# Kernel tuning notes

Hardware: AMD Instinct MI355X
Metric: run time of the kernel (lower is better)

Reference implementation:

```python
import jax, jax.numpy as jnp
import numpy as np

N_NODES = 50000
N_EDGES = 500000
N_REL = 8
D = 128        # input_dim
A_DIM = 64     # attention_dim
D_OUT = 128    # output_dim


def setup_inputs() -> dict:
    key = jax.random.key(0)
    ks = jax.random.split(key, 10)
    h = jax.random.normal(ks[0], (N_NODES, D), jnp.float32)
    # relation gate tables: [R, 2*D, D]; first D rows act on dst (subject), last D on src (object)
    relations = jax.random.normal(ks[1], (N_REL, 2 * D, D), jnp.float32) * 0.05
    rel_attention = jax.random.normal(ks[2], (N_REL, A_DIM), jnp.float32) * 0.05
    W_a = jax.random.normal(ks[3], (A_DIM, 2 * D), jnp.float32) * 0.05
    b_a = jnp.zeros((A_DIM,), jnp.float32)
    W_lin = jax.random.normal(ks[4], (D_OUT, 2 * D), jnp.float32) * 0.05
    b_lin = jnp.zeros((D_OUT,), jnp.float32)
    src = jax.random.randint(ks[5], (N_EDGES,), 0, N_NODES, dtype=jnp.int32)
    dst = jax.random.randint(ks[6], (N_EDGES,), 0, N_NODES, dtype=jnp.int32)
    etype = jax.random.randint(ks[7], (N_EDGES,), 0, N_REL, dtype=jnp.int32)
    return {"h": h, "relations": relations, "rel_attention": rel_attention,
            "W_a": W_a, "b_a": b_a, "W_lin": W_lin, "b_lin": b_lin,
            "src": src, "dst": dst, "etype": etype}


def reference(h, relations, rel_attention, W_a, b_a, W_lin, b_lin, src, dst, etype):
    d = h.shape[-1]
    # --- gates: relation-indexed gather_mm (concat gate type) ---
    # Project every node through every relation once (R is small), then gather per edge.
    proj_dst = jnp.einsum('nd,rde->rne', h, relations[:, :d, :])   # [R, N, D] subject/dst side
    proj_src = jnp.einsum('nd,rde->rne', h, relations[:, d:, :])   # [R, N, D] object/src side
    gate = jax.nn.sigmoid(proj_dst[etype, dst] + proj_src[etype, src])  # [E, D]

    src_h = h[src]   # [E, D]
    dst_h = h[dst]   # [E, D]

    # --- gatv2 attention (predicates are zeroed in the module -> rel_attention[0]) ---
    a = jax.nn.leaky_relu(jnp.concatenate([dst_h, src_h], axis=-1) @ W_a.T + b_a)  # [E, A]
    score = (rel_attention[0] * a).sum(-1)  # [E]

    # --- edge_softmax over destination-node segments ---
    smax = jax.ops.segment_max(score, dst, num_segments=N_NODES)
    ex = jnp.exp(score - smax[dst])
    denom = jax.ops.segment_sum(ex, dst, num_segments=N_NODES)
    attn = ex / denom[dst]  # [E]

    # --- message = u_mul_e(h, attn*gate), reduce = sum over dst ---
    msg = src_h * (attn[:, None] * gate)                 # [E, D]
    h_N = jax.ops.segment_sum(msg, dst, num_segments=N_NODES)  # [N, D]

    # --- graphsage aggregate: LeakyReLU(W [h ; h_N] + b) ---
    out = jax.nn.leaky_relu(jnp.concatenate([h, h_N], axis=-1) @ W_lin.T + b_lin)
    return out
```

## Files before the change

### kernel.cpp

```cpp
#include <hip/hip_runtime.h>
#include <cstdint>
#include <cstddef>

constexpr int NNODES = 50000;
constexpr int NEDGES = 500000;
constexpr int NRELS  = 8;
constexpr int DIM    = 128;
constexpr int ADIM   = 64;
constexpr int TWOD   = 256;
constexpr int EPB    = 64;
constexpr float SLOPE = 0.01f;

constexpr int XPITCH = TWOD + 8;
constexpr int SPAD = NEDGES + 1024;

typedef __attribute__((ext_vector_type(8))) short short8;
typedef __attribute__((ext_vector_type(4))) float floatx4;

__device__ __forceinline__ unsigned short f2bf(float f) {
    unsigned u = __float_as_uint(f);
    unsigned r = u + 0x7FFFu + ((u >> 16) & 1u);
    return (unsigned short)(r >> 16);
}
__device__ __forceinline__ float bf2f(unsigned short b) {
    return __uint_as_float(((unsigned)b) << 16);
}
__device__ __forceinline__ float sigmoid_fast(float x) {
    return __builtin_amdgcn_rcpf(1.0f + __expf(-x));
}

__global__ void k_init(int* __restrict__ histD, int* __restrict__ cursorD,
                       int* __restrict__ cnts) {
    int i = blockIdx.x * blockDim.x + threadIdx.x;
    int stride = gridDim.x * blockDim.x;
    for (int idx = i; idx < NNODES; idx += stride) { histD[idx] = 0; cursorD[idx] = 0; }
    if (i < 16) cnts[i] = 0;
}

__global__ __launch_bounds__(256) void k_prep(const float* __restrict__ rel,
                                              const float* __restrict__ W_lin,
                                              const float* __restrict__ W_a,
                                              unsigned short* __restrict__ relT,
                                              unsigned short* __restrict__ Wl,
                                              unsigned short* __restrict__ Wa16) {
    __shared__ float ls[64][65];
    int b = blockIdx.x, t = threadIdx.x;
    if (b < 64) {
        int r = b >> 3, tile = b & 7;
        int d0 = (tile >> 1) * 64, o0 = (tile & 1) * 64;
        const float* rp = rel + ((size_t)r * TWOD + d0) * DIM + o0;
#pragma unroll
        for (int u = 0; u < 16; u++) {
            int v = u * 256 + t;
            int j = v & 63, i = v >> 6;
            ls[i][j] = rp[(size_t)i * DIM + j];
        }
        __syncthreads();
        unsigned short* wp = relT + ((size_t)r * DIM + o0) * TWOD + d0;
#pragma unroll
        for (int u = 0; u < 16; u++) {
            int v = u * 256 + t;
            int ii = v & 63, jj = v >> 6;
            wp[(size_t)jj * TWOD + ii] = f2bf(ls[ii][jj]);
        }
    } else {
        int idx = (b - 64) * 256 + t;
        if (idx < DIM * TWOD) {
            Wl[idx] = f2bf(W_lin[idx]);
        } else {
            int j = idx - DIM * TWOD;
            if (j < ADIM * TWOD) Wa16[j] = f2bf(W_a[j]);
        }
    }
}

__global__ void k_h16(const float* __restrict__ h, unsigned short* __restrict__ h16) {
    int i = blockIdx.x * 256 + threadIdx.x;
    if (i < NNODES * DIM / 8) {
        const float4* hp = (const float4*)(h + (size_t)i * 8);
        float4 a = hp[0], b = hp[1];
        union { unsigned short us[8]; short8 s8; } pk;
        pk.us[0] = f2bf(a.x); pk.us[1] = f2bf(a.y); pk.us[2] = f2bf(a.z); pk.us[3] = f2bf(a.w);
        pk.us[4] = f2bf(b.x); pk.us[5] = f2bf(b.y); pk.us[6] = f2bf(b.z); pk.us[7] = f2bf(b.w);
        *(short8*)&h16[(size_t)i * 8] = pk.s8;
    }
}

__global__ void k_hist2(const int* __restrict__ ety, const int* __restrict__ dst,
                        int* __restrict__ cnt, int* __restrict__ histD) {
    __shared__ int hist[NRELS];
    int t = threadIdx.x;
    if (t < NRELS) hist[t] = 0;
    __syncthreads();
    int e = blockIdx.x * 256 + t;
    if (e < NEDGES) {
        atomicAdd(&hist[ety[e]], 1);
        atomicAdd(&histD[dst[e]], 1);
    }
    __syncthreads();
    if (t < NRELS && hist[t] > 0) atomicAdd(&cnt[t], hist[t]);
}

__global__ __launch_bounds__(1024) void k_scan(const int* __restrict__ histD,
                                               int* __restrict__ row_ptr,
                                               const int* __restrict__ cnt,
                                               int* __restrict__ offs,
                                               uint2* __restrict__ sMeta) {
    __shared__ int ls[1024];
    __shared__ int s_offs[NRELS + 1];
    __shared__ int s_cnt[NRELS];
    const int t = threadIdx.x;
    const int CH = (NNODES + 1023) / 1024;
    const int base = t * CH;
    int s = 0;
    for (int j = 0; j < CH; j++) { int i = base + j; if (i < NNODES) s += histD[i]; }
    ls[t] = s;
    __syncthreads();
    for (int off = 1; off < 1024; off <<= 1) {
        int v = (t >= off) ? ls[t - off] : 0;
        __syncthreads();
        ls[t] += v;
        __syncthreads();
    }
    int run = (t == 0) ? 0 : ls[t - 1];
    for (int j = 0; j < CH; j++) {
        int i = base + j;
        if (i < NNODES) { row_ptr[i] = run; run += histD[i]; }
    }
    if (t == 1023) row_ptr[NNODES] = ls[1023];
    if (t == 0) {
        int off = 0;
        for (int r = 0; r < NRELS; r++) {
            offs[r] = off; s_offs[r] = off; s_cnt[r] = cnt[r];
            off += ((cnt[r] + EPB - 1) / EPB) * EPB;
        }
        s_offs[NRELS] = off;
    }
    __syncthreads();
#pragma unroll
    for (int r = 0; r < NRELS; r++) {
        int s0 = s_offs[r] + s_cnt[r];
        int e0 = s_offs[r + 1 > NRELS ? NRELS : r + 1];
        for (int idx = s0 + t; idx < e0; idx += 1024) sMeta[idx] = make_uint2(0xFFFFFFFFu, 0u);
    }
    for (int idx = s_offs[NRELS] + t; idx < SPAD; idx += 1024)
        sMeta[idx] = make_uint2(0xFFFFFFFFu, 0u);
}

__global__ void k_escatter(const int* __restrict__ ety, const int* __restrict__ src,
                           const int* __restrict__ dst, const int* __restrict__ row_ptr,
                           const int* __restrict__ offs,
                           int* __restrict__ cursorD, int* __restrict__ cursorE,
                           uint2* __restrict__ sMeta) {
    __shared__ int hist[NRELS];
    __shared__ int basew[NRELS];
    int t = threadIdx.x;
    if (t < NRELS) hist[t] = 0;
    __syncthreads();
    int e = blockIdx.x * 256 + t;
    int r = -1, rank = 0, sn = 0, dn = 0;
    if (e < NEDGES) {
        r = ety[e]; sn = src[e]; dn = dst[e];
        rank = atomicAdd(&hist[r], 1);
    }
    __syncthreads();
    if (t < NRELS && hist[t] > 0) basew[t] = atomicAdd(&cursorE[t], hist[t]);
    __syncthreads();
    if (e < NEDGES) {
        int s = offs[r] + basew[r] + rank;
        int pos = row_ptr[dn] + atomicAdd(&cursorD[dn], 1);
        sMeta[s] = make_uint2((unsigned)sn | ((unsigned)dn << 16), (unsigned)pos);
    }
}

__global__ __launch_bounds__(256, 5) void k_gate_msg(
    const unsigned short* __restrict__ h16, const unsigned short* __restrict__ relT,
    const unsigned short* __restrict__ Wa16,
    const uint2* __restrict__ sMeta, const float* __restrict__ b_a,
    const float* __restrict__ ratt, const int* __restrict__ offs,
    unsigned short* __restrict__ msgbuf, float* __restrict__ scoreP) {
    __shared__ unsigned short Xs[EPB * 256];

    const int t = threadIdx.x;
    const int base = blockIdx.x * EPB;
    const int lane = t & 63;
    const int wave = t >> 6;

    uint2 sm = sMeta[base + lane];
    const unsigned smx = sm.x;
    const unsigned smy = sm.y;

    if (__shfl((int)smx, 0) == -1) return;

    int r = 0;
#pragma unroll
    for (int i = 1; i < NRELS; i++) if (base >= offs[i]) r = i;

#pragma unroll
    for (int u = 0; u < 8; u++) {
        int i = u * 8 + (t >> 5);
        int c = t & 31;
        unsigned x = (unsigned)__shfl((int)smx, i);
        int node = (x == 0xFFFFFFFFu) ? 0 : ((c < 16) ? (int)(x >> 16) : (int)(x & 0xFFFFu));
        *(short8*)&Xs[i * 256 + ((c ^ (i & 7)) << 3)] =
            *(const short8*)&h16[(size_t)node * DIM + (c & 15) * 8];
    }

    const int q = lane >> 4;
    const int l16 = lane & 15;
    const int o16 = wave * 16 + l16;

    const unsigned short* bp0 = relT + ((size_t)r * DIM + (wave * 2 + 0) * 16 + l16) * TWOD + q * 8;
    const unsigned short* bp1 = relT + ((size_t)r * DIM + (wave * 2 + 1) * 16 + l16) * TWOD + q * 8;
    const unsigned short* wb  = Wa16 + (size_t)o16 * TWOD + q * 8;

    __syncthreads();

    floatx4 acc[4][2];
    floatx4 accS[4];
#pragma unroll
    for (int m = 0; m < 4; m++) {
        acc[m][0] = (floatx4)(0.0f);
        acc[m][1] = (floatx4)(0.0f);
        accS[m] = (floatx4)(0.0f);
    }

#pragma unroll
    for (int ks = 0; ks < 8; ks++) {
        short8 B0 = *(const short8*)(bp0 + ks * 32);
        short8 B1 = *(const short8*)(bp1 + ks * 32);
        short8 BS = *(const short8*)(wb + ks * 32);
        short8 Af[4];
#pragma unroll
        for (int m = 0; m < 4; m++) {
            int row = m * 16 + l16;
            Af[m] = *(const short8*)&Xs[row * 256 + ((((ks * 4) + q) ^ (l16 & 7)) << 3)];
        }
#pragma unroll
        for (int m = 0; m < 4; m++) {
            acc[m][0] = __builtin_amdgcn_mfma_f32_16x16x32_bf16(Af[m], B0, acc[m][0], 0, 0, 0);
            acc[m][1] = __builtin_amdgcn_mfma_f32_16x16x32_bf16(Af[m], B1, acc[m][1], 0, 0, 0);
            accS[m]   = __builtin_amdgcn_mfma_f32_16x16x32_bf16(Af[m], BS, accS[m], 0, 0, 0);
        }
    }

    __syncthreads();

#pragma unroll
    for (int m = 0; m < 4; m++) {
        int ib = m * 16 + q * 4;
#pragma unroll
        for (int nn = 0; nn < 2; nn++) {
            int o = (wave * 2 + nn) * 16 + l16;
            int uS = 16 + (o >> 3), uD = o >> 3, ofs = o & 7;
#pragma unroll
            for (int rg = 0; rg < 4; rg++) {
                int i = ib + rg;
                float g = sigmoid_fast(acc[m][nn][rg]);
                float sh = bf2f(Xs[i * 256 + ((uS ^ (i & 7)) << 3) + ofs]);
                Xs[i * 256 + ((uD ^ (i & 7)) << 3) + ofs] = f2bf(sh * g);
            }
        }
    }
    __syncthreads();

    {
        float ba = b_a[o16];
        float ra = ratt[o16];
#pragma unroll
        for (int m = 0; m < 4; m++) {
#pragma unroll
            for (int rg = 0; rg < 4; rg++) {
                float v = accS[m][rg] + ba;
                v = v > 0.0f ? v : SLOPE * v;
                v *= ra;
#pragma unroll
                for (int off = 8; off > 0; off >>= 1) v += __shfl_xor(v, off, 16);
                if (l16 == 0) ((float*)&Xs[(m * 16 + q * 4 + rg) * 256 + 128])[wave] = v;
            }
        }
    }

#pragma unroll
    for (int u = 0; u < 4; u++) {
        int i = u * 16 + (t >> 4);
        int c = t & 15;
        unsigned x = (unsigned)__shfl((int)smx, i);
        unsigned pos = (unsigned)__shfl((int)smy, i);
        if (x == 0xFFFFFFFFu) continue;
        short8 val = *(const short8*)&Xs[i * 256 + ((c ^ (i & 7)) << 3)];
        *(short8*)&msgbuf[(size_t)pos * DIM + c * 8] = val;
    }
    __syncthreads();

    if (t < EPB && smx != 0xFFFFFFFFu) {
        const float* sw = (const float*)&Xs[t * 256 + 128];
        scoreP[smy] = sw[0] + sw[1] + sw[2] + sw[3];
    }
}

__global__ __launch_bounds__(256) void k_aggr(const unsigned short* __restrict__ msgbuf,
                                              const float* __restrict__ scoreP,
                                              const int* __restrict__ row_ptr,
                                              unsigned short* __restrict__ hN16) {
    int n = blockIdx.x * 4 + (threadIdx.x >> 6);
    int lane = threadIdx.x & 63;
    if (n >= NNODES) return;
    int p0 = row_ptr[n], p1 = row_ptr[n + 1];
    float a0 = 0.0f, a1 = 0.0f;
    if (p0 < p1) {
        float mx = -3.0e38f;
        for (int p = p0 + lane; p < p1; p += 64) mx = fmaxf(mx, scoreP[p]);
#pragma unroll
        for (int off = 32; off > 0; off >>= 1) mx = fmaxf(mx, __shfl_xor(mx, off));
        float sum = 0.0f;
        for (int p = p0 + lane; p < p1; p += 64) sum += __expf(scoreP[p] - mx);
#pragma unroll
        for (int off = 32; off > 0; off >>= 1) sum += __shfl_xor(sum, off);
        int p = p0;
        const unsigned short* mb = msgbuf + (size_t)lane * 2;
        for (; p + 4 <= p1; p += 4) {
            float w0 = __expf(scoreP[p + 0] - mx);
            float w1 = __expf(scoreP[p + 1] - mx);
            float w2 = __expf(scoreP[p + 2] - mx);
            float w3 = __expf(scoreP[p + 3] - mx);
            unsigned v0 = *(const unsigned*)&mb[(size_t)(p + 0) * DIM];
            unsigned v1 = *(const unsigned*)&mb[(size_t)(p + 1) * DIM];
            unsigned v2 = *(const unsigned*)&mb[(size_t)(p + 2) * DIM];
            unsigned v3 = *(const unsigned*)&mb[(size_t)(p + 3) * DIM];
            a0 = fmaf(w0, bf2f((unsigned short)(v0 & 0xFFFFu)), a0);
            a1 = fmaf(w0, bf2f((unsigned short)(v0 >> 16)), a1);
            a0 = fmaf(w1, bf2f((unsigned short)(v1 & 0xFFFFu)), a0);
            a1 = fmaf(w1, bf2f((unsigned short)(v1 >> 16)), a1);
            a0 = fmaf(w2, bf2f((unsigned short)(v2 & 0xFFFFu)), a0);
            a1 = fmaf(w2, bf2f((unsigned short)(v2 >> 16)), a1);
            a0 = fmaf(w3, bf2f((unsigned short)(v3 & 0xFFFFu)), a0);
            a1 = fmaf(w3, bf2f((unsigned short)(v3 >> 16)), a1);
        }
        for (; p < p1; p++) {
            float w = __expf(scoreP[p] - mx);
            unsigned v = *(const unsigned*)&mb[(size_t)p * DIM];
            a0 = fmaf(w, bf2f((unsigned short)(v & 0xFFFFu)), a0);
            a1 = fmaf(w, bf2f((unsigned short)(v >> 16)), a1);
        }
        float inv = __builtin_amdgcn_rcpf(sum);
        a0 *= inv; a1 *= inv;
    }
    unsigned o = (unsigned)f2bf(a0) | ((unsigned)f2bf(a1) << 16);
    *(unsigned*)&hN16[(size_t)n * DIM + lane * 2] = o;
}

__global__ __launch_bounds__(256) void k_out(const unsigned short* __restrict__ h16,
                                             const unsigned short* __restrict__ hN16,
                                             const unsigned short* __restrict__ Wl,
                                             const float* __restrict__ b_lin,
                                             float* __restrict__ out) {
    __shared__ unsigned short Xs[EPB * XPITCH];
    const int t = threadIdx.x;
    const int nb = blockIdx.x * 64;

#pragma unroll
    for (int u = 0; u < 8; u++) {
        int v = u * 256 + t;
        int i = v >> 5;
        int c = v & 31;
        int n = nb + i;
        if (n >= NNODES) n = NNODES - 1;
        const unsigned short* srcp = (c < 16) ? h16 : hN16;
        *(short8*)&Xs[i * XPITCH + c * 8] = *(const short8*)&srcp[(size_t)n * DIM + (c & 15) * 8];
    }

    const int wave = t >> 6;
    const int lane = t & 63;
    const int q = lane >> 4;
    const int l16 = lane & 15;

    short8 Bf[2][8];
#pragma unroll
    for (int nn = 0; nn < 2; nn++) {
        int o = (wave * 2 + nn) * 16 + l16;
        const unsigned short* bp = Wl + (size_t)o * TWOD + q * 8;
#pragma unroll
        for (int ks = 0; ks < 8; ks++) Bf[nn][ks] = *(const short8*)(bp + ks * 32);
    }

    __syncthreads();

    floatx4 acc[4][2];
#pragma unroll
    for (int m = 0; m < 4; m++)
#pragma unroll
        for (int nn = 0; nn < 2; nn++) acc[m][nn] = (floatx4)(0.0f);

#pragma unroll
    for (int ks = 0; ks < 8; ks++) {
        short8 Af[4];
        const unsigned short* xb = &Xs[l16 * XPITCH + ks * 32 + q * 8];
#pragma unroll
        for (int m = 0; m < 4; m++) Af[m] = *(const short8*)(xb + m * 16 * XPITCH);
#pragma unroll
        for (int m = 0; m < 4; m++)
#pragma unroll
            for (int nn = 0; nn < 2; nn++)
                acc[m][nn] = __builtin_amdgcn_mfma_f32_16x16x32_bf16(Af[m], Bf[nn][ks], acc[m][nn], 0, 0, 0);
    }

#pragma unroll
    for (int m = 0; m < 4; m++) {
        int ib = m * 16 + q * 4;
#pragma unroll
        for (int nn = 0; nn < 2; nn++) {
            int o = (wave * 2 + nn) * 16 + l16;
            float bl = b_lin[o];
#pragma unroll
            for (int rg = 0; rg < 4; rg++) {
                int n = nb + ib + rg;
                if (n < NNODES) {
                    float val = acc[m][nn][rg] + bl;
                    val = val > 0.0f ? val : SLOPE * val;
                    out[(size_t)n * DIM + o] = val;
                }
            }
        }
    }
}

extern "C" void kernel_launch(void* const* d_in, const int* in_sizes, int n_in,
                              void* d_out, int out_size, void* d_ws, size_t ws_size,
                              hipStream_t stream) {
    const float* h     = (const float*)d_in[0];
    const float* rel   = (const float*)d_in[1];
    const float* ratt  = (const float*)d_in[2];
    const float* W_a   = (const float*)d_in[3];
    const float* b_a   = (const float*)d_in[4];
    const float* W_lin = (const float*)d_in[5];
    const float* b_lin = (const float*)d_in[6];
    const int* src = (const int*)d_in[7];
    const int* dst = (const int*)d_in[8];
    const int* ety = (const int*)d_in[9];
    float* out = (float*)d_out;

    float* scoreP = (float*)d_ws;
    unsigned short* h16  = (unsigned short*)(scoreP + NEDGES);
    unsigned short* hN16 = h16 + (size_t)NNODES * DIM;
    unsigned short* relT = hN16 + (size_t)NNODES * DIM;
    unsigned short* Wl   = relT + (size_t)NRELS * DIM * TWOD;
    unsigned short* Wa16 = Wl + (size_t)DIM * TWOD;
    uint2* sMeta = (uint2*)(Wa16 + (size_t)ADIM * TWOD);
    int* row_ptr = (int*)(sMeta + SPAD);
    int* histD   = row_ptr + (NNODES + 1);
    int* cursorD = histD + NNODES;
    int* cnts    = cursorD + NNODES;
    int* offs    = cnts + 16;
    unsigned short* msgbuf = (unsigned short*)(((uintptr_t)(offs + 8) + 255) & ~(uintptr_t)255);

    k_init<<<256, 256, 0, stream>>>(histD, cursorD, cnts);
    k_prep<<<64 + (DIM * TWOD + ADIM * TWOD + 255) / 256, 256, 0, stream>>>(
        rel, W_lin, W_a, relT, Wl, Wa16);
    k_h16<<<(NNODES * DIM / 8 + 255) / 256, 256, 0, stream>>>(h, h16);
    k_hist2<<<(NEDGES + 255) / 256, 256, 0, stream>>>(ety, dst, cnts, histD);
    k_scan<<<1, 1024, 0, stream>>>(histD, row_ptr, cnts, offs, sMeta);
    k_escatter<<<(NEDGES + 255) / 256, 256, 0, stream>>>(
        ety, src, dst, row_ptr, offs, cursorD, cnts + 8, sMeta);
    k_gate_msg<<<(NEDGES + 8 * EPB + EPB - 1) / EPB, 256, 0, stream>>>(
        h16, relT, Wa16, sMeta, b_a, ratt, offs, msgbuf, scoreP);
    k_aggr<<<(NNODES + 3) / 4, 256, 0, stream>>>(msgbuf, scoreP, row_ptr, hN16);
    k_out<<<(NNODES + 63) / 64, 256, 0, stream>>>(h16, hN16, Wl, b_lin, out);
}
```

Before: 459.1 us.

## Prefetch relation weights, reload edge metadata instead of shuffles, move cursor reset

In the gate/message kernel, the first four k-steps of relation and attention weight fragments are loaded before the barrier so their latency overlaps the shared-memory fill. Per-lane shuffles of edge metadata are replaced with direct global loads of sMeta. The message store loop is re-indexed to a flat thread mapping. Separately, the cursorD reset moves from k_init into the scan kernel, and k_init's grid shrinks. The prefetch costs extra registers, and the duplicated sMeta loads add memory traffic.

After: 539.6 us. +17.5%, slower.

```diff
diff --git a/kernel.cpp b/kernel.cpp
--- a/kernel.cpp
+++ b/kernel.cpp
@@ -13,6 +13,7 @@
 
 constexpr int XPITCH = TWOD + 8;
 constexpr int SPAD = NEDGES + 1024;
+constexpr int NGRP = (NEDGES + 8 * EPB + EPB - 1) / EPB;
 
 typedef __attribute__((ext_vector_type(8))) short short8;
 typedef __attribute__((ext_vector_type(4))) float floatx4;
@@ -29,11 +30,10 @@
     return __builtin_amdgcn_rcpf(1.0f + __expf(-x));
 }
 
-__global__ void k_init(int* __restrict__ histD, int* __restrict__ cursorD,
-                       int* __restrict__ cnts) {
+__global__ void k_init(int* __restrict__ histD, int* __restrict__ cnts) {
     int i = blockIdx.x * blockDim.x + threadIdx.x;
     int stride = gridDim.x * blockDim.x;
-    for (int idx = i; idx < NNODES; idx += stride) { histD[idx] = 0; cursorD[idx] = 0; }
+    for (int idx = i; idx < NNODES; idx += stride) histD[idx] = 0;
     if (i < 16) cnts[i] = 0;
 }
 
@@ -103,6 +103,7 @@
 
 __global__ __launch_bounds__(1024) void k_scan(const int* __restrict__ histD,
                                                int* __restrict__ row_ptr,
+                                               int* __restrict__ cursorD,
                                                const int* __restrict__ cnt,
                                                int* __restrict__ offs,
                                                uint2* __restrict__ sMeta) {
@@ -125,7 +126,7 @@
     int run = (t == 0) ? 0 : ls[t - 1];
     for (int j = 0; j < CH; j++) {
         int i = base + j;
-        if (i < NNODES) { row_ptr[i] = run; run += histD[i]; }
+        if (i < NNODES) { row_ptr[i] = run; cursorD[i] = 0; run += histD[i]; }
     }
     if (t == 1023) row_ptr[NNODES] = ls[1023];
     if (t == 0) {
@@ -186,21 +187,21 @@
     const int lane = t & 63;
     const int wave = t >> 6;
 
-    uint2 sm = sMeta[base + lane];
-    const unsigned smx = sm.x;
-    const unsigned smy = sm.y;
-
-    if (__shfl((int)smx, 0) == -1) return;
+    if (sMeta[base].x == 0xFFFFFFFFu) return;
 
     int r = 0;
 #pragma unroll
     for (int i = 1; i < NRELS; i++) if (base >= offs[i]) r = i;
 
+    const int i0 = t >> 5;
+    const int c  = t & 31;
+    unsigned mg[8];
+#pragma unroll
+    for (int u = 0; u < 8; u++) mg[u] = sMeta[base + u * 8 + i0].x;
 #pragma unroll
     for (int u = 0; u < 8; u++) {
-        int i = u * 8 + (t >> 5);
-        int c = t & 31;
-        unsigned x = (unsigned)__shfl((int)smx, i);
+        int i = u * 8 + i0;
+        unsigned x = mg[u];
         int node = (x == 0xFFFFFFFFu) ? 0 : ((c < 16) ? (int)(x >> 16) : (int)(x & 0xFFFFu));
         *(short8*)&Xs[i * 256 + ((c ^ (i & 7)) << 3)] =
             *(const short8*)&h16[(size_t)node * DIM + (c & 15) * 8];
@@ -213,6 +214,14 @@
     const unsigned short* bp0 = relT + ((size_t)r * DIM + (wave * 2 + 0) * 16 + l16) * TWOD + q * 8;
     const unsigned short* bp1 = relT + ((size_t)r * DIM + (wave * 2 + 1) * 16 + l16) * TWOD + q * 8;
     const unsigned short* wb  = Wa16 + (size_t)o16 * TWOD + q * 8;
+
+    short8 B0p[4], B1p[4], BSp[4];
+#pragma unroll
+    for (int ks = 0; ks < 4; ks++) {
+        B0p[ks] = *(const short8*)(bp0 + ks * 32);
+        B1p[ks] = *(const short8*)(bp1 + ks * 32);
+        BSp[ks] = *(const short8*)(wb + ks * 32);
+    }
 
     __syncthreads();
 
@@ -227,9 +236,9 @@
 
 #pragma unroll
     for (int ks = 0; ks < 8; ks++) {
-        short8 B0 = *(const short8*)(bp0 + ks * 32);
-        short8 B1 = *(const short8*)(bp1 + ks * 32);
-        short8 BS = *(const short8*)(wb + ks * 32);
+        short8 B0 = (ks < 4) ? B0p[ks & 3] : *(const short8*)(bp0 + ks * 32);
+        short8 B1 = (ks < 4) ? B1p[ks & 3] : *(const short8*)(bp1 + ks * 32);
+        short8 BS = (ks < 4) ? BSp[ks & 3] : *(const short8*)(wb + ks * 32);
         short8 Af[4];
 #pragma unroll
         for (int m = 0; m < 4; m++) {
@@ -283,19 +292,22 @@
 
 #pragma unroll
     for (int u = 0; u < 4; u++) {
-        int i = u * 16 + (t >> 4);
-        int c = t & 15;
-        unsigned x = (unsigned)__shfl((int)smx, i);
-        unsigned pos = (unsigned)__shfl((int)smy, i);
-        if (x == 0xFFFFFFFFu) continue;
-        short8 val = *(const short8*)&Xs[i * 256 + ((c ^ (i & 7)) << 3)];
-        *(short8*)&msgbuf[(size_t)pos * DIM + c * 8] = val;
-    }
-    __syncthreads();
-
-    if (t < EPB && smx != 0xFFFFFFFFu) {
-        const float* sw = (const float*)&Xs[t * 256 + 128];
-        scoreP[smy] = sw[0] + sw[1] + sw[2] + sw[3];
+        int v = u * 256 + t;
+        int i = v >> 4;
+        int cc = v & 15;
+        uint2 m2 = sMeta[base + i];
+        if (m2.x == 0xFFFFFFFFu) continue;
+        short8 val = *(const short8*)&Xs[i * 256 + ((cc ^ (i & 7)) << 3)];
+        *(short8*)&msgbuf[(size_t)m2.y * DIM + cc * 8] = val;
+    }
+    __syncthreads();
+
+    if (t < EPB) {
+        uint2 m2 = sMeta[base + t];
+        if (m2.x != 0xFFFFFFFFu) {
+            const float* sw = (const float*)&Xs[t * 256 + 128];
+            scoreP[m2.y] = sw[0] + sw[1] + sw[2] + sw[3];
+        }
     }
 }
 
@@ -454,15 +466,15 @@
     int* offs    = cnts + 16;
     unsigned short* msgbuf = (unsigned short*)(((uintptr_t)(offs + 8) + 255) & ~(uintptr_t)255);
 
-    k_init<<<256, 256, 0, stream>>>(histD, cursorD, cnts);
+    k_init<<<196, 256, 0, stream>>>(histD, cnts);
     k_prep<<<64 + (DIM * TWOD + ADIM * TWOD + 255) / 256, 256, 0, stream>>>(
         rel, W_lin, W_a, relT, Wl, Wa16);
     k_h16<<<(NNODES * DIM / 8 + 255) / 256, 256, 0, stream>>>(h, h16);
     k_hist2<<<(NEDGES + 255) / 256, 256, 0, stream>>>(ety, dst, cnts, histD);
-    k_scan<<<1, 1024, 0, stream>>>(histD, row_ptr, cnts, offs, sMeta);
+    k_scan<<<1, 1024, 0, stream>>>(histD, row_ptr, cursorD, cnts, offs, sMeta);
     k_escatter<<<(NEDGES + 255) / 256, 256, 0, stream>>>(
         ety, src, dst, row_ptr, offs, cursorD, cnts + 8, sMeta);
-    k_gate_msg<<<(NEDGES + 8 * EPB + EPB - 1) / EPB, 256, 0, stream>>>(
+    k_gate_msg<<<NGRP, 256, 0, stream>>>(
         h16, relT, Wa16, sMeta, b_a, ratt, offs, msgbuf, scoreP);
     k_aggr<<<(NNODES + 3) / 4, 256, 0, stream>>>(msgbuf, scoreP, row_ptr, hN16);
     k_out<<<(NNODES + 63) / 64, 256, 0, stream>>>(h16, hN16, Wl, b_lin, out);
```
